# Optimization experiments

Measured on AMD Instinct MI355X. Metric: run time of the kernel, lower is better.

Reference implementation:

```python
import jax, jax.numpy as jnp
import numpy as np

EMBED = 1024
HEADS = 16
HEAD_DIM = EMBED // HEADS


def setup_inputs() -> dict:
    key = jax.random.key(0)
    ks = jax.random.split(key, 10)
    B, S = 2, 2048
    x = jax.random.normal(ks[0], (B, S, EMBED), dtype=jnp.float32)
    s = 1.0 / np.sqrt(EMBED)
    Wq = jax.random.normal(ks[1], (EMBED, EMBED), dtype=jnp.float32) * s
    Wk = jax.random.normal(ks[2], (EMBED, EMBED), dtype=jnp.float32) * s
    Wv = jax.random.normal(ks[3], (EMBED, EMBED), dtype=jnp.float32) * s
    Wo = jax.random.normal(ks[4], (EMBED, EMBED), dtype=jnp.float32) * s
    bq = jnp.zeros((EMBED,), jnp.float32)
    bk = jnp.zeros((EMBED,), jnp.float32)
    bv = jnp.zeros((EMBED,), jnp.float32)
    bo = jnp.zeros((EMBED,), jnp.float32)
    J = jax.random.normal(ks[5], (HEADS, HEAD_DIM, HEAD_DIM), dtype=jnp.float32) * 0.02
    lam = jnp.asarray(0.5, jnp.float32)
    return {"x": x, "Wq": Wq, "bq": bq, "Wk": Wk, "bk": bk,
            "Wv": Wv, "bv": bv, "Wo": Wo, "bo": bo, "J": J, "lam": lam}


def reference(x, Wq, bq, Wk, bk, Wv, bv, Wo, bo, J, lam):
    B, S, E = x.shape
    H, hd = HEADS, HEAD_DIM
    scale = np.sqrt(hd).astype(np.float32)

    def split_heads(t):  # (B,S,E) -> (B,H,S,hd)
        return t.reshape(B, S, H, hd).transpose(0, 2, 1, 3)

    Q = split_heads(x @ Wq + bq)
    K = split_heads(x @ Wk + bk)
    V = split_heads(x @ Wv + bv)

    scores = jnp.einsum('bhid,bhjd->bhij', Q, K) / scale
    Qn = jnp.tanh(Q)
    Kn = jnp.tanh(K)
    # bilinear correction: tanh(Q) J tanh(K)^T per head
    delta = jnp.einsum('bhid,hde,bhje->bhij', Qn, J, Kn)
    scores = scores + lam * delta

    causal = jnp.triu(jnp.ones((S, S), dtype=bool), k=1)  # True above diagonal
    scores = jnp.where(causal[None, None], -jnp.inf, scores)

    probs = jax.nn.softmax(scores, axis=-1)
    out = jnp.einsum('bhij,bhjd->bhid', probs, V)
    out = out.transpose(0, 2, 1, 3).reshape(B, S, E)
    return out @ Wo + bo
```

## Files before the change

### kernel.cpp

```cpp
#include <hip/hip_runtime.h>
#include <cstdint>
#include <cstddef>

typedef __bf16 bf16x8 __attribute__((ext_vector_type(8)));
typedef short  s16x8  __attribute__((ext_vector_type(8)));
typedef float  f32x4  __attribute__((ext_vector_type(4)));
typedef unsigned int u32x4 __attribute__((ext_vector_type(4)));

#define MFMA16(a, b, c) __builtin_amdgcn_mfma_f32_16x16x32_bf16((a), (b), (c), 0, 0, 0)

typedef __attribute__((address_space(3))) unsigned int       lds_uint;
typedef const __attribute__((address_space(1))) unsigned int glb_uint;

static __device__ __forceinline__ void gload_lds16(const void* g, void* l) {
  __builtin_amdgcn_global_load_lds((glb_uint*)g, (lds_uint*)l, 16, 0, 0);
}

static __device__ __forceinline__ unsigned short f2bf(float f) {
  unsigned u = __builtin_bit_cast(unsigned, f);
  unsigned r = u + 0x7FFFu + ((u >> 16) & 1u);
  return (unsigned short)(r >> 16);
}
static __device__ __forceinline__ float bf2f(unsigned short u) {
  unsigned x = ((unsigned)u) << 16;
  return __builtin_bit_cast(float, x);
}
static __device__ __forceinline__ float fast_tanh(float x) {
  float e = __expf(2.f * x);
  return 1.f - 2.f / (e + 1.f);
}
static __device__ __forceinline__ unsigned cvt_pk_bf16(float lo, float hi) {
  unsigned r;
  asm("v_cvt_pk_bf16_f32 %0, %1, %2" : "=v"(r) : "v"(lo), "v"(hi));
  return r;
}

__global__ void k_f32_to_bf16(const float* __restrict__ src,
                              unsigned short* __restrict__ dst, int n4) {
  int i = blockIdx.x * blockDim.x + threadIdx.x;
  if (i >= n4) return;
  float4 v = reinterpret_cast<const float4*>(src)[i];
  ushort4 o;
  o.x = f2bf(v.x); o.y = f2bf(v.y); o.z = f2bf(v.z); o.w = f2bf(v.w);
  reinterpret_cast<ushort4*>(dst)[i] = o;
}

__global__ void k_transpose4_to_bf16(const float* __restrict__ s0,
                                     const float* __restrict__ s1,
                                     const float* __restrict__ s2,
                                     const float* __restrict__ s3,
                                     unsigned short* __restrict__ dstBase) {
  __shared__ float t[32][33];
  const int z = blockIdx.z;
  const float* src = (z == 0) ? s0 : (z == 1) ? s1 : (z == 2) ? s2 : s3;
  unsigned short* dst = dstBase + (size_t)z * 1048576;
  int c0 = blockIdx.x * 32, r0 = blockIdx.y * 32;
  int tx = threadIdx.x, ty = threadIdx.y;
#pragma unroll
  for (int i = 0; i < 4; ++i)
    t[ty + i * 8][tx] = src[(size_t)(r0 + ty + i * 8) * 1024 + c0 + tx];
  __syncthreads();
#pragma unroll
  for (int i = 0; i < 4; ++i)
    dst[(size_t)(c0 + ty + i * 8) * 1024 + r0 + tx] = f2bf(t[tx][ty + i * 8]);
}

template <int MODE>
__global__ __launch_bounds__(256) void k_gemm(
    const unsigned short* __restrict__ A, const unsigned short* __restrict__ Bt,
    int M, int N, int K,
    float* __restrict__ Cout, const float* __restrict__ bias) {
  __shared__ __align__(16) unsigned short Al[128 * 64];
  __shared__ __align__(16) unsigned short Bl[128 * 64];
  const int tid = threadIdx.x;
  const int lane = tid & 63, w = tid >> 6;
  const int wm = w >> 1, wn = w & 1;
  const int l15 = lane & 15, l4 = lane >> 4;
  const int m0 = blockIdx.y * 128, n0 = blockIdx.x * 128;

  const int srow = lane >> 3;
  const int schunk = (lane & 7) ^ srow;
  const unsigned short* Ag = A + (size_t)(m0 + (w << 5) + srow) * K + (schunk << 3);
  const unsigned short* Bg = Bt + (size_t)(n0 + (w << 5) + srow) * K + (schunk << 3);
  unsigned short* Alw = Al + (w << 5) * 64;
  unsigned short* Blw = Bl + (w << 5) * 64;

  const f32x4 zero4 = {0.f, 0.f, 0.f, 0.f};
  f32x4 acc[4][4];
#pragma unroll
  for (int i = 0; i < 4; ++i)
#pragma unroll
    for (int j = 0; j < 4; ++j) acc[i][j] = zero4;

  for (int k0 = 0; k0 < K; k0 += 64) {
#pragma unroll
    for (int p = 0; p < 4; ++p) {
      gload_lds16(Ag + (size_t)(p * 8) * K + k0, Alw + p * 8 * 64);
      gload_lds16(Bg + (size_t)(p * 8) * K + k0, Blw + p * 8 * 64);
    }
    __syncthreads();
#pragma unroll
    for (int c = 0; c < 2; ++c) {
      bf16x8 af[4], bfr[4];
#pragma unroll
      for (int i = 0; i < 4; ++i) {
        int ra = wm * 64 + i * 16 + l15;
        af[i] = *reinterpret_cast<const bf16x8*>(
            reinterpret_cast<const char*>(Al) + ra * 128 +
            ((c * 64 + l4 * 16) ^ ((ra & 7) << 4)));
        int rb = wn * 64 + i * 16 + l15;
        bfr[i] = *reinterpret_cast<const bf16x8*>(
            reinterpret_cast<const char*>(Bl) + rb * 128 +
            ((c * 64 + l4 * 16) ^ ((rb & 7) << 4)));
      }
#pragma unroll
      for (int i = 0; i < 4; ++i)
#pragma unroll
        for (int j = 0; j < 4; ++j) acc[i][j] = MFMA16(af[i], bfr[j], acc[i][j]);
    }
    __syncthreads();
  }

#pragma unroll
  for (int i = 0; i < 4; ++i)
#pragma unroll
    for (int j = 0; j < 4; ++j)
#pragma unroll
      for (int r = 0; r < 4; ++r) {
        int mrow = m0 + wm * 64 + i * 16 + l4 * 4 + r;
        int ncol = n0 + wn * 64 + j * 16 + l15;
        Cout[(size_t)mrow * N + ncol] = acc[i][j][r] + bias[ncol];
      }
}

__global__ __launch_bounds__(512, 2) void k_gemm256_qkv(
    const unsigned short* __restrict__ A, const unsigned short* __restrict__ Bt,
    int M, int N, int K,
    const float* __restrict__ bq, const float* __restrict__ bk,
    const float* __restrict__ bv,
    unsigned short* __restrict__ Qa, unsigned short* __restrict__ Ka,
    unsigned short* __restrict__ Vt, unsigned short* __restrict__ Qn) {
  __shared__ __align__(16) unsigned short Al[2][256 * 64];
  __shared__ __align__(16) unsigned short Bl[2][256 * 64];
  const int tid = threadIdx.x;
  const int lane = tid & 63;
  const int w = tid >> 6, wm = w >> 2, wn = w & 3;
  const int l15 = lane & 15, l4 = lane >> 4;
  const int nbx = N >> 8;
  const int bid = (int)blockIdx.x;
  const int lin = (bid & 7) * ((int)gridDim.x >> 3) + (bid >> 3);
  const int m0 = (lin / nbx) << 8, n0 = (lin % nbx) << 8;
  const int NT = K >> 6;

  const int strow = tid >> 3, stchunk = tid & 7;
  const int schunk = stchunk ^ (strow & 7);

  auto stage = [&](int slot, int kt, int hh) {
    const unsigned short* src = (hh < 2) ? A : Bt;
    const int base0 = (hh < 2) ? m0 : n0;
    unsigned short* dst = (hh < 2) ? &Al[slot][0] : &Bl[slot][0];
    const int hrow = (hh & 1) * 128;
#pragma unroll
    for (int i = 0; i < 2; ++i) {
      int row = hrow + i * 64 + strow;
      gload_lds16(src + (size_t)(base0 + row) * K + kt * 64 + schunk * 8,
                  dst + row * 64 + stchunk * 8);
    }
  };

  const f32x4 zero4 = {0.f, 0.f, 0.f, 0.f};
  f32x4 acc[8][4];
#pragma unroll
  for (int i = 0; i < 8; ++i)
#pragma unroll
    for (int j = 0; j < 4; ++j) acc[i][j] = zero4;

  stage(0, 0, 0); stage(0, 0, 1); stage(0, 0, 2); stage(0, 0, 3);
  stage(1, 1, 0); stage(1, 1, 1); stage(1, 1, 2); stage(1, 1, 3);
  asm volatile("s_waitcnt vmcnt(8)" ::: "memory");
  __builtin_amdgcn_s_barrier();

  bf16x8 af[4][2], bf0[2][2], bf1[2][2];

  for (int kt = 0; kt < NT; ++kt) {
    const int s = kt & 1;
    const char* As = (const char*)&Al[s][0];
    const char* Bs = (const char*)&Bl[s][0];
    const int kp2 = (kt + 2 < NT) ? kt + 2 : NT - 1;

#pragma unroll
    for (int i = 0; i < 4; ++i) {
      const int ra = wm * 128 + i * 16 + l15;
#pragma unroll
      for (int kk = 0; kk < 2; ++kk)
        af[i][kk] = *(const bf16x8*)(As + ra * 128 + (((kk * 4 + l4) ^ (ra & 7)) << 4));
    }
#pragma unroll
    for (int j = 0; j < 2; ++j) {
      const int rb = wn * 64 + j * 16 + l15;
#pragma unroll
      for (int kk = 0; kk < 2; ++kk)
        bf0[j][kk] = *(const bf16x8*)(Bs + rb * 128 + (((kk * 4 + l4) ^ (rb & 7)) << 4));
    }
    __builtin_amdgcn_s_barrier();
    __builtin_amdgcn_s_setprio(1);
#pragma unroll
    for (int i = 0; i < 4; ++i)
#pragma unroll
      for (int j = 0; j < 2; ++j)
#pragma unroll
        for (int kk = 0; kk < 2; ++kk)
          acc[i][j] = MFMA16(af[i][kk], bf0[j][kk], acc[i][j]);
    __builtin_amdgcn_s_setprio(0);
    __builtin_amdgcn_s_barrier();

#pragma unroll
    for (int j = 0; j < 2; ++j) {
      const int rb = wn * 64 + (2 + j) * 16 + l15;
#pragma unroll
      for (int kk = 0; kk < 2; ++kk)
        bf1[j][kk] = *(const bf16x8*)(Bs + rb * 128 + (((kk * 4 + l4) ^ (rb & 7)) << 4));
    }
    __builtin_amdgcn_s_barrier();
    __builtin_amdgcn_s_setprio(1);
#pragma unroll
    for (int i = 0; i < 4; ++i)
#pragma unroll
      for (int j = 0; j < 2; ++j)
#pragma unroll
        for (int kk = 0; kk < 2; ++kk)
          acc[i][2 + j] = MFMA16(af[i][kk], bf1[j][kk], acc[i][2 + j]);
    __builtin_amdgcn_s_setprio(0);
    __builtin_amdgcn_s_barrier();

#pragma unroll
    for (int i = 0; i < 4; ++i) {
      const int ra = wm * 128 + (4 + i) * 16 + l15;
#pragma unroll
      for (int kk = 0; kk < 2; ++kk)
        af[i][kk] = *(const bf16x8*)(As + ra * 128 + (((kk * 4 + l4) ^ (ra & 7)) << 4));
    }
    __builtin_amdgcn_s_barrier();
    __builtin_amdgcn_s_setprio(1);
#pragma unroll
    for (int i = 0; i < 4; ++i)
#pragma unroll
      for (int j = 0; j < 2; ++j)
#pragma unroll
        for (int kk = 0; kk < 2; ++kk)
          acc[4 + i][2 + j] = MFMA16(af[i][kk], bf1[j][kk], acc[4 + i][2 + j]);
    __builtin_amdgcn_s_setprio(0);
    __builtin_amdgcn_s_barrier();

    stage(s, kp2, 0); stage(s, kp2, 1); stage(s, kp2, 2); stage(s, kp2, 3);
    __builtin_amdgcn_s_setprio(1);
#pragma unroll
    for (int i = 0; i < 4; ++i)
#pragma unroll
      for (int j = 0; j < 2; ++j)
#pragma unroll
        for (int kk = 0; kk < 2; ++kk)
          acc[4 + i][j] = MFMA16(af[i][kk], bf0[j][kk], acc[4 + i][j]);
    __builtin_amdgcn_s_setprio(0);
    asm volatile("s_waitcnt vmcnt(8)" ::: "memory");
    __builtin_amdgcn_s_barrier();
  }
  asm volatile("s_waitcnt vmcnt(0)" ::: "memory");

#pragma unroll
  for (int mf = 0; mf < 8; ++mf) {
#pragma unroll
    for (int nf = 0; nf < 4; ++nf) {
#pragma unroll
      for (int r = 0; r < 4; ++r) {
        const int mrow = m0 + wm * 128 + mf * 16 + l4 * 4 + r;
        const int ncol = n0 + wn * 64 + nf * 16 + l15;
        const float v = acc[mf][nf][r];
        const int proj = ncol >> 10, nn = ncol & 1023;
        const int h = nn >> 6, d = nn & 63;
        const int b = mrow >> 11, sq = mrow & 2047;
        const size_t t64 = (size_t)(b * 16 + h) * 2048 + sq;
        if (proj == 0) {
          float q = v + bq[nn];
          Qa[t64 * 128 + d] = f2bf(q * 0.125f);
          Qn[t64 * 64 + d] = f2bf(fast_tanh(q));
        } else if (proj == 1) {
          float kk = v + bk[nn];
          Ka[t64 * 128 + d] = f2bf(kk);
          Ka[t64 * 128 + 64 + d] = f2bf(fast_tanh(kk));
        } else {
          Vt[((size_t)(b * 16 + h) * 64 + d) * 2048 + sq] = f2bf(v + bv[nn]);
        }
      }
    }
  }
}

__global__ __launch_bounds__(256) void k_qnj(const unsigned short* __restrict__ Qn,
                                             const float* __restrict__ J,
                                             const float* __restrict__ lamPtr,
                                             unsigned short* __restrict__ Qa) {
  __shared__ float Jl[64 * 64];
  __shared__ float Ql[64 * 64];
  int bid = blockIdx.x;
  int bh = bid >> 5, sblk = bid & 31;
  int h = bh & 15;
  int tid = threadIdx.x;
  float lam = lamPtr[0];
  const float4* Jh = reinterpret_cast<const float4*>(J + (size_t)h * 4096);
#pragma unroll
  for (int p = 0; p < 4; ++p)
    reinterpret_cast<float4*>(Jl)[p * 256 + tid] = Jh[p * 256 + tid];
  size_t tok0 = (size_t)bh * 2048 + sblk * 64;
#pragma unroll
  for (int p = 0; p < 2; ++p) {
    int idx = p * 256 + tid;
    s16x8 v = *reinterpret_cast<const s16x8*>(Qn + tok0 * 64 + idx * 8);
#pragma unroll
    for (int j = 0; j < 8; ++j) Ql[idx * 8 + j] = bf2f((unsigned short)v[j]);
  }
  __syncthreads();
  int e = tid & 63, wq = tid >> 6;
#pragma unroll 1
  for (int pass = 0; pass < 16; ++pass) {
    int tok = pass * 4 + wq;
    float a0 = 0.f, a1 = 0.f;
#pragma unroll
    for (int d = 0; d < 64; d += 2) {
      a0 += Ql[tok * 64 + d] * Jl[d * 64 + e];
      a1 += Ql[tok * 64 + d + 1] * Jl[(d + 1) * 64 + e];
    }
    Qa[(tok0 + tok) * 128 + 64 + e] = f2bf(lam * (a0 + a1));
  }
}

__global__ __launch_bounds__(256) void k_attn(const unsigned short* __restrict__ Qa,
                                              const unsigned short* __restrict__ Ka,
                                              const unsigned short* __restrict__ Vt,
                                              unsigned short* __restrict__ Ob) {
  constexpr int S = 2048;
  __shared__ __align__(16) unsigned short Klds[2][64 * 128];
  __shared__ __align__(16) unsigned short Vtl[2][64 * 64];

  const int blk = (int)blockIdx.x;
  const int xg = blk & 7, idx = blk >> 3;
  const int bh = xg * 4 + (idx & 3);
  const int qt = 31 - (idx >> 2);
  const int b = bh >> 4, h = bh & 15;
  const int tid = threadIdx.x;
  const int lane = tid & 63, w = tid >> 6;
  const int l15 = lane & 15, l4 = lane >> 4;
  const int q0 = qt * 64;
  const size_t bhS = (size_t)bh * S;
  const unsigned short* Kbase = Ka + bhS * 128;
  const unsigned short* Vbase = Vt + (size_t)bh * 64 * 2048;
  const f32x4 zero4 = {0.f, 0.f, 0.f, 0.f};

  const int rowbase = w * 16 + (lane >> 4);
  const int rb7 = rowbase & 7;
  const int cK0 = (lane & 15) ^ rb7;
  const int cK1 = cK0 ^ 4;
  const int vdvrow = w * 16 + (lane >> 3);
  const int cV = (lane & 7) ^ ((lane >> 3) & 7);

  bf16x8 qf[4];
  {
    int qrow = q0 + w * 16 + l15;
#pragma unroll
    for (int c = 0; c < 4; ++c)
      qf[c] = *reinterpret_cast<const bf16x8*>(Qa + (bhS + qrow) * 128 + c * 32 + l4 * 8);
  }

  f32x4 oacc[4];
  float m_ = -__builtin_inff(), lsum = 0.f;
#pragma unroll
  for (int v = 0; v < 4; ++v) oacc[v] = zero4;

  const int I0 = (l15 + 32 * (l4 & 1)) * 4;
  const int I1 = I0 + 64;
  const bool hi4 = (lane & 32) != 0;

#pragma unroll
  for (int p = 0; p < 4; ++p)
    gload_lds16(Kbase + (size_t)(rowbase + 4 * p) * 128 + ((p & 1) ? cK1 : cK0) * 8,
                &Klds[0][(w * 16 + p * 4) * 128]);
#pragma unroll
  for (int p = 0; p < 2; ++p)
    gload_lds16(Vbase + (size_t)(vdvrow + 8 * p) * 2048 + cV * 8,
                &Vtl[0][(w * 16 + p * 8) * 64]);
  __syncthreads();

  for (int kt = 0; kt <= qt; ++kt) {
    const int cur = kt & 1;
    const bool lastStep = (kt == qt);

    if (!lastStep) {
      const int base = (kt + 1) * 64;
      const int nxt = cur ^ 1;
#pragma unroll
      for (int p = 0; p < 4; ++p)
        gload_lds16(Kbase + (size_t)(base + rowbase + 4 * p) * 128 + ((p & 1) ? cK1 : cK0) * 8,
                    &Klds[nxt][(w * 16 + p * 4) * 128]);
#pragma unroll
      for (int p = 0; p < 2; ++p)
        gload_lds16(Vbase + (size_t)(vdvrow + 8 * p) * 2048 + base + cV * 8,
                    &Vtl[nxt][(w * 16 + p * 8) * 64]);
    }

    const char* Kl = reinterpret_cast<const char*>(Klds[cur]);
    f32x4 sc[4];
    __builtin_amdgcn_s_setprio(1);
#pragma unroll
    for (int fn = 0; fn < 4; ++fn) {
      sc[fn] = zero4;
      const int krow = fn * 16 + l15;
#pragma unroll
      for (int c = 0; c < 4; ++c) {
        bf16x8 kf = *reinterpret_cast<const bf16x8*>(
            Kl + krow * 256 + (((c * 4 + l4) ^ (krow & 7)) << 4));
        sc[fn] = MFMA16(kf, qf[c], sc[fn]);
      }
    }
    __builtin_amdgcn_s_setprio(0);

    if (lastStep) {
      const int qloc = w * 16 + l15;
#pragma unroll
      for (int fn = 0; fn < 4; ++fn)
#pragma unroll
        for (int r = 0; r < 4; ++r)
          if (fn * 16 + l4 * 4 + r > qloc) sc[fn][r] = -__builtin_inff();
    }

    float mx = sc[0][0];
#pragma unroll
    for (int fn = 0; fn < 4; ++fn)
#pragma unroll
      for (int r = 0; r < 4; ++r) mx = fmaxf(mx, sc[fn][r]);
    mx = fmaxf(mx, __shfl_xor(mx, 16));
    mx = fmaxf(mx, __shfl_xor(mx, 32));
    const float mn = fmaxf(m_, mx);
    const float al = __expf(m_ - mn);
    float p_[4][4];
    float rs = 0.f;
#pragma unroll
    for (int fn = 0; fn < 4; ++fn)
#pragma unroll
      for (int r = 0; r < 4; ++r) {
        float e = __expf(sc[fn][r] - mn);
        p_[fn][r] = e;
        rs += e;
      }
    rs += __shfl_xor(rs, 16);
    rs += __shfl_xor(rs, 32);
    lsum = lsum * al + rs;
    m_ = mn;

#pragma unroll
    for (int r = 0; r < 4; ++r) {
      float albc = __shfl(al, l4 * 4 + r);
#pragma unroll
      for (int v = 0; v < 4; ++v) oacc[v][r] *= albc;
    }

    unsigned cp[4][2];
#pragma unroll
    for (int fn = 0; fn < 4; ++fn) {
      cp[fn][0] = cvt_pk_bf16(p_[fn][0], p_[fn][1]);
      cp[fn][1] = cvt_pk_bf16(p_[fn][2], p_[fn][3]);
    }

    const char* Vl = reinterpret_cast<const char*>(Vtl[cur]);
#pragma unroll
    for (int c2 = 0; c2 < 2; ++c2) {
      unsigned a0 = __builtin_amdgcn_ds_bpermute(I0, (int)cp[c2 * 2][0]);
      unsigned b0 = __builtin_amdgcn_ds_bpermute(I0, (int)cp[c2 * 2 + 1][0]);
      unsigned a1 = __builtin_amdgcn_ds_bpermute(I0, (int)cp[c2 * 2][1]);
      unsigned b1 = __builtin_amdgcn_ds_bpermute(I0, (int)cp[c2 * 2 + 1][1]);
      unsigned a2 = __builtin_amdgcn_ds_bpermute(I1, (int)cp[c2 * 2][0]);
      unsigned b2 = __builtin_amdgcn_ds_bpermute(I1, (int)cp[c2 * 2 + 1][0]);
      unsigned a3 = __builtin_amdgcn_ds_bpermute(I1, (int)cp[c2 * 2][1]);
      unsigned b3 = __builtin_amdgcn_ds_bpermute(I1, (int)cp[c2 * 2 + 1][1]);
      u32x4 pw = {hi4 ? b0 : a0, hi4 ? b1 : a1, hi4 ? b2 : a2, hi4 ? b3 : a3};
      bf16x8 pa = __builtin_bit_cast(bf16x8, pw);
      __builtin_amdgcn_s_setprio(1);
#pragma unroll
      for (int v = 0; v < 4; ++v) {
        const int dvrow = v * 16 + l15;
        bf16x8 vf = *reinterpret_cast<const bf16x8*>(
            Vl + dvrow * 128 + (((c2 * 4 + l4) ^ (dvrow & 7)) << 4));
        oacc[v] = MFMA16(pa, vf, oacc[v]);
      }
      __builtin_amdgcn_s_setprio(0);
    }

    __syncthreads();
  }

  float lbc[4];
#pragma unroll
  for (int r = 0; r < 4; ++r) lbc[r] = __shfl(lsum, l4 * 4 + r);
#pragma unroll
  for (int v = 0; v < 4; ++v) {
#pragma unroll
    for (int r = 0; r < 4; ++r) {
      int row = q0 + w * 16 + l4 * 4 + r;
      float o = oacc[v][r] / lbc[r];
      Ob[((size_t)b * S + row) * 1024 + h * 64 + v * 16 + l15] = f2bf(o);
    }
  }
}

extern "C" void kernel_launch(void* const* d_in, const int* in_sizes, int n_in,
                              void* d_out, int out_size, void* d_ws, size_t ws_size,
                              hipStream_t stream) {
  const float* x   = (const float*)d_in[0];
  const float* Wq  = (const float*)d_in[1];
  const float* bq  = (const float*)d_in[2];
  const float* Wk  = (const float*)d_in[3];
  const float* bk  = (const float*)d_in[4];
  const float* Wv  = (const float*)d_in[5];
  const float* bv  = (const float*)d_in[6];
  const float* Wo  = (const float*)d_in[7];
  const float* bo  = (const float*)d_in[8];
  const float* J   = (const float*)d_in[9];
  const float* lam = (const float*)d_in[10];
  float* out = (float*)d_out;

  char* ws = (char*)d_ws;
  unsigned short* xb     = (unsigned short*)(ws);
  unsigned short* Wt_qkv = (unsigned short*)(ws + 8388608);
  unsigned short* Wt_o   = (unsigned short*)(ws + 14680064);
  unsigned short* Qa     = (unsigned short*)(ws + 16777216);
  unsigned short* Ka     = (unsigned short*)(ws + 33554432);
  unsigned short* Vt     = (unsigned short*)(ws + 50331648);
  unsigned short* Qn     = (unsigned short*)(ws + 58720256);
  unsigned short* Ob     = (unsigned short*)(ws + 67108864);

  k_f32_to_bf16<<<4096, 256, 0, stream>>>(x, xb, 1048576);

  k_transpose4_to_bf16<<<dim3(32, 32, 4), dim3(32, 8), 0, stream>>>(
      Wq, Wk, Wv, Wo, Wt_qkv);

  k_gemm256_qkv<<<192, 512, 0, stream>>>(xb, Wt_qkv, 4096, 3072, 1024,
      bq, bk, bv, Qa, Ka, Vt, Qn);

  k_qnj<<<1024, 256, 0, stream>>>(Qn, J, lam, Qa);

  k_attn<<<1024, 256, 0, stream>>>(Qa, Ka, Vt, Ob);

  k_gemm<0><<<dim3(8, 32), 256, 0, stream>>>(Ob, Wt_o, 4096, 1024, 1024,
      out, bo);
}
```

Measured before the change: 195.1 us.

## Double-buffer output GEMM and simplify QKV GEMM pipeline to one-ahead prefetch

The output-projection GEMM gains double-buffered LDS, so the next K tile is fetched while the current one feeds MFMAs, and MFMA blocks are raised to higher priority. The QKV GEMM drops its prefetch-two-ahead scheme, fine-grained barriers and manual vmcnt waits, and moves to a one-ahead prefetch with a single __syncthreads per iteration. This trades fewer barriers for a shorter prefetch distance, which may expose more global-load latency in the QKV GEMM.

```diff
diff --git a/kernel.cpp b/kernel.cpp
--- a/kernel.cpp
+++ b/kernel.cpp
@@ -65,25 +65,33 @@
     dst[(size_t)(c0 + ty + i * 8) * 1024 + r0 + tx] = f2bf(t[tx][ty + i * 8]);
 }
 
-template <int MODE>
-__global__ __launch_bounds__(256) void k_gemm(
+__global__ __launch_bounds__(256) void k_gemm_op(
     const unsigned short* __restrict__ A, const unsigned short* __restrict__ Bt,
     int M, int N, int K,
     float* __restrict__ Cout, const float* __restrict__ bias) {
-  __shared__ __align__(16) unsigned short Al[128 * 64];
-  __shared__ __align__(16) unsigned short Bl[128 * 64];
+  __shared__ __align__(16) unsigned short Al[2][128 * 64];
+  __shared__ __align__(16) unsigned short Bl[2][128 * 64];
   const int tid = threadIdx.x;
   const int lane = tid & 63, w = tid >> 6;
   const int wm = w >> 1, wn = w & 1;
   const int l15 = lane & 15, l4 = lane >> 4;
   const int m0 = blockIdx.y * 128, n0 = blockIdx.x * 128;
+  const int NT = K >> 6;
 
   const int srow = lane >> 3;
   const int schunk = (lane & 7) ^ srow;
   const unsigned short* Ag = A + (size_t)(m0 + (w << 5) + srow) * K + (schunk << 3);
   const unsigned short* Bg = Bt + (size_t)(n0 + (w << 5) + srow) * K + (schunk << 3);
-  unsigned short* Alw = Al + (w << 5) * 64;
-  unsigned short* Blw = Bl + (w << 5) * 64;
+
+  auto stage = [&](int slot, int t) {
+    unsigned short* Alw = &Al[slot][0] + (w << 5) * 64;
+    unsigned short* Blw = &Bl[slot][0] + (w << 5) * 64;
+#pragma unroll
+    for (int p = 0; p < 4; ++p) {
+      gload_lds16(Ag + (size_t)(p * 8) * K + t * 64, Alw + p * 8 * 64);
+      gload_lds16(Bg + (size_t)(p * 8) * K + t * 64, Blw + p * 8 * 64);
+    }
+  };
 
   const f32x4 zero4 = {0.f, 0.f, 0.f, 0.f};
   f32x4 acc[4][4];
@@ -92,13 +100,15 @@
 #pragma unroll
     for (int j = 0; j < 4; ++j) acc[i][j] = zero4;
 
-  for (int k0 = 0; k0 < K; k0 += 64) {
-#pragma unroll
-    for (int p = 0; p < 4; ++p) {
-      gload_lds16(Ag + (size_t)(p * 8) * K + k0, Alw + p * 8 * 64);
-      gload_lds16(Bg + (size_t)(p * 8) * K + k0, Blw + p * 8 * 64);
-    }
-    __syncthreads();
+  stage(0, 0);
+  __syncthreads();
+
+  for (int t = 0; t < NT; ++t) {
+    const int s = t & 1;
+    const int tn = (t + 1 < NT) ? t + 1 : NT - 1;
+    stage(s ^ 1, tn);
+    const char* As = (const char*)&Al[s][0];
+    const char* Bs = (const char*)&Bl[s][0];
 #pragma unroll
     for (int c = 0; c < 2; ++c) {
       bf16x8 af[4], bfr[4];
@@ -106,17 +116,17 @@
       for (int i = 0; i < 4; ++i) {
         int ra = wm * 64 + i * 16 + l15;
         af[i] = *reinterpret_cast<const bf16x8*>(
-            reinterpret_cast<const char*>(Al) + ra * 128 +
-            ((c * 64 + l4 * 16) ^ ((ra & 7) << 4)));
+            As + ra * 128 + ((c * 64 + l4 * 16) ^ ((ra & 7) << 4)));
         int rb = wn * 64 + i * 16 + l15;
         bfr[i] = *reinterpret_cast<const bf16x8*>(
-            reinterpret_cast<const char*>(Bl) + rb * 128 +
-            ((c * 64 + l4 * 16) ^ ((rb & 7) << 4)));
+            Bs + rb * 128 + ((c * 64 + l4 * 16) ^ ((rb & 7) << 4)));
       }
+      __builtin_amdgcn_s_setprio(1);
 #pragma unroll
       for (int i = 0; i < 4; ++i)
 #pragma unroll
         for (int j = 0; j < 4; ++j) acc[i][j] = MFMA16(af[i], bfr[j], acc[i][j]);
+      __builtin_amdgcn_s_setprio(0);
     }
     __syncthreads();
   }
@@ -155,16 +165,14 @@
   const int strow = tid >> 3, stchunk = tid & 7;
   const int schunk = stchunk ^ (strow & 7);
 
-  auto stage = [&](int slot, int kt, int hh) {
-    const unsigned short* src = (hh < 2) ? A : Bt;
-    const int base0 = (hh < 2) ? m0 : n0;
-    unsigned short* dst = (hh < 2) ? &Al[slot][0] : &Bl[slot][0];
-    const int hrow = (hh & 1) * 128;
-#pragma unroll
-    for (int i = 0; i < 2; ++i) {
-      int row = hrow + i * 64 + strow;
-      gload_lds16(src + (size_t)(base0 + row) * K + kt * 64 + schunk * 8,
-                  dst + row * 64 + stchunk * 8);
+  auto stage = [&](int slot, int kt) {
+#pragma unroll
+    for (int i = 0; i < 4; ++i) {
+      int row = i * 64 + strow;
+      gload_lds16(A + (size_t)(m0 + row) * K + kt * 64 + schunk * 8,
+                  &Al[slot][0] + row * 64 + stchunk * 8);
+      gload_lds16(Bt + (size_t)(n0 + row) * K + kt * 64 + schunk * 8,
+                  &Bl[slot][0] + row * 64 + stchunk * 8);
     }
   };
 
@@ -175,10 +183,8 @@
 #pragma unroll
     for (int j = 0; j < 4; ++j) acc[i][j] = zero4;
 
-  stage(0, 0, 0); stage(0, 0, 1); stage(0, 0, 2); stage(0, 0, 3);
-  stage(1, 1, 0); stage(1, 1, 1); stage(1, 1, 2); stage(1, 1, 3);
-  asm volatile("s_waitcnt vmcnt(8)" ::: "memory");
-  __builtin_amdgcn_s_barrier();
+  stage(0, 0);
+  __syncthreads();
 
   bf16x8 af[4][2], bf0[2][2], bf1[2][2];
 
@@ -186,7 +192,9 @@
     const int s = kt & 1;
     const char* As = (const char*)&Al[s][0];
     const char* Bs = (const char*)&Bl[s][0];
-    const int kp2 = (kt + 2 < NT) ? kt + 2 : NT - 1;
+    const int kp1 = (kt + 1 < NT) ? kt + 1 : NT - 1;
+
+    stage(s ^ 1, kp1);
 
 #pragma unroll
     for (int i = 0; i < 4; ++i) {
@@ -202,7 +210,6 @@
       for (int kk = 0; kk < 2; ++kk)
         bf0[j][kk] = *(const bf16x8*)(Bs + rb * 128 + (((kk * 4 + l4) ^ (rb & 7)) << 4));
     }
-    __builtin_amdgcn_s_barrier();
     __builtin_amdgcn_s_setprio(1);
 #pragma unroll
     for (int i = 0; i < 4; ++i)
@@ -212,7 +219,6 @@
         for (int kk = 0; kk < 2; ++kk)
           acc[i][j] = MFMA16(af[i][kk], bf0[j][kk], acc[i][j]);
     __builtin_amdgcn_s_setprio(0);
-    __builtin_amdgcn_s_barrier();
 
 #pragma unroll
     for (int j = 0; j < 2; ++j) {
@@ -221,7 +227,6 @@
       for (int kk = 0; kk < 2; ++kk)
         bf1[j][kk] = *(const bf16x8*)(Bs + rb * 128 + (((kk * 4 + l4) ^ (rb & 7)) << 4));
     }
-    __builtin_amdgcn_s_barrier();
     __builtin_amdgcn_s_setprio(1);
 #pragma unroll
     for (int i = 0; i < 4; ++i)
@@ -231,7 +236,6 @@
         for (int kk = 0; kk < 2; ++kk)
           acc[i][2 + j] = MFMA16(af[i][kk], bf1[j][kk], acc[i][2 + j]);
     __builtin_amdgcn_s_setprio(0);
-    __builtin_amdgcn_s_barrier();
 
 #pragma unroll
     for (int i = 0; i < 4; ++i) {
@@ -240,7 +244,6 @@
       for (int kk = 0; kk < 2; ++kk)
         af[i][kk] = *(const bf16x8*)(As + ra * 128 + (((kk * 4 + l4) ^ (ra & 7)) << 4));
     }
-    __builtin_amdgcn_s_barrier();
     __builtin_amdgcn_s_setprio(1);
 #pragma unroll
     for (int i = 0; i < 4; ++i)
@@ -249,11 +252,7 @@
 #pragma unroll
         for (int kk = 0; kk < 2; ++kk)
           acc[4 + i][2 + j] = MFMA16(af[i][kk], bf1[j][kk], acc[4 + i][2 + j]);
-    __builtin_amdgcn_s_setprio(0);
-    __builtin_amdgcn_s_barrier();
-
-    stage(s, kp2, 0); stage(s, kp2, 1); stage(s, kp2, 2); stage(s, kp2, 3);
-    __builtin_amdgcn_s_setprio(1);
+
 #pragma unroll
     for (int i = 0; i < 4; ++i)
 #pragma unroll
@@ -262,10 +261,9 @@
         for (int kk = 0; kk < 2; ++kk)
           acc[4 + i][j] = MFMA16(af[i][kk], bf0[j][kk], acc[4 + i][j]);
     __builtin_amdgcn_s_setprio(0);
-    asm volatile("s_waitcnt vmcnt(8)" ::: "memory");
-    __builtin_amdgcn_s_barrier();
-  }
-  asm volatile("s_waitcnt vmcnt(0)" ::: "memory");
+
+    __syncthreads();
+  }
 
 #pragma unroll
   for (int mf = 0; mf < 8; ++mf) {
@@ -549,6 +547,6 @@
 
   k_attn<<<1024, 256, 0, stream>>>(Qa, Ka, Vt, Ob);
 
-  k_gemm<0><<<dim3(8, 32), 256, 0, stream>>>(Ob, Wt_o, 4096, 1024, 1024,
+  k_gemm_op<<<dim3(8, 32), 256, 0, stream>>>(Ob, Wt_o, 4096, 1024, 1024,
       out, bo);
 }
```

Result: no change. 195.4 us (+0.2%).
